# Optimization experiments

Measured on AMD Instinct MI355X. Metric: run time of the kernel, lower is better.

Reference implementation:

```python
import jax, jax.numpy as jnp
import numpy as np

NUM_GROUPS = 8
ROUTING_ITERS = 3
EPS = 1e-8

def setup_inputs() -> dict:
    key = jax.random.key(0)
    ks = jax.random.split(key, 6)
    B, C, H, W = 16, 256, 64, 64
    Cq = C // 4
    G = NUM_GROUPS
    x = jax.random.normal(ks[0], (B, C, H, W), jnp.float32)
    group_assignments = jax.random.uniform(ks[1], (B, C, G), jnp.float32)
    conv_w = jax.random.normal(ks[2], (Cq, C), jnp.float32) * 0.05
    conv_b = jax.random.normal(ks[3], (Cq,), jnp.float32) * 0.05
    lin_w = jax.random.normal(ks[4], (C * G, Cq), jnp.float32) * 0.05
    lin_b = jax.random.normal(ks[5], (C * G,), jnp.float32) * 0.05
    return {"x": x, "group_assignments": group_assignments,
            "conv_w": conv_w, "conv_b": conv_b, "lin_w": lin_w, "lin_b": lin_b}

def reference(x, group_assignments, conv_w, conv_b, lin_w, lin_b):
    B, C, H, W = x.shape
    G = NUM_GROUPS
    # routing_predictor: 1x1 conv (pure channel mix) -> ReLU -> global avg pool -> linear
    h = jax.nn.relu(jnp.einsum('bchw,dc->bdhw', x, conv_w) + conv_b[None, :, None, None])
    pooled = h.mean(axis=(2, 3))                               # (B, C//4)
    logits = (pooled @ lin_w.T + lin_b).reshape(B, C, G)       # (B, C, G)
    logits = logits + jnp.log(group_assignments + EPS)
    xf = x.reshape(B, C, H * W)                                # (B, C, N)
    x_norm = jnp.maximum(jnp.linalg.norm(xf, axis=2), EPS)     # (B, C)
    # dynamic routing: last iteration's softmax/group-sum contributes nothing to output,
    # so only ROUTING_ITERS-1 agreement updates are applied (same math as torch code)
    for _ in range(ROUTING_ITERS - 1):
        w = jax.nn.softmax(logits, axis=-1)                    # (B, C, G)
        s = jnp.einsum('bcg,bcn->bgn', w, xf)                  # group outputs (B, G, N)
        s_norm = jnp.maximum(jnp.linalg.norm(s, axis=2), EPS)  # (B, G)
        sim = jnp.einsum('bcn,bgn->bcg', xf, s) / (x_norm[:, :, None] * s_norm[:, None, :])
        logits = logits + sim
    final_weights = jax.nn.softmax(logits, axis=-1)
    return final_weights, x
```

## Files before the change

### kernel.cpp

```cpp
#include <hip/hip_runtime.h>

#define BB 16
#define CC 256
#define NN 4096
#define CN (CC*NN)
#define GG 8
#define EPSF 1e-8f
#define NT 64

typedef __attribute__((ext_vector_type(8))) short bf16x8;
typedef __attribute__((ext_vector_type(4))) float f32x4;
typedef __attribute__((ext_vector_type(2))) unsigned int uint32x2;

__device__ __forceinline__ unsigned short bfr(float f) {
  unsigned int u = __float_as_uint(f);
  return (unsigned short)((u + 0x7FFFu + ((u >> 16) & 1u)) >> 16);
}

__global__ __launch_bounds__(512, 2) void k_prep(const float* __restrict__ x,
                                                 const float* __restrict__ conv_w,
                                                 const float* __restrict__ conv_b,
                                                 float* __restrict__ xout,
                                                 float* __restrict__ xnp,
                                                 float* __restrict__ pooledpart,
                                                 unsigned short* __restrict__ xbf_g) {
  const int b = blockIdx.x >> 6;
  const int chunk = blockIdx.x & 63;
  const int t = threadIdx.x;
  const int lane = t & 63, wv = t >> 6;
  __shared__ unsigned short xbf[16384];
  __shared__ float pool[8 * 16];

  const int dt = wv >> 1, h2 = wv & 1;
  const int g = lane >> 4, col = lane & 15;
  const int drow = dt * 16 + col;
  union AF { uint4 q; bf16x8 v; unsigned short u[8]; } a[8];
  {
    const float* wrow = conv_w + (size_t)drow * 256;
#pragma unroll
    for (int kk = 0; kk < 8; ++kk) {
      float4 w0 = *(const float4*)(wrow + kk * 32 + g * 8);
      float4 w1 = *(const float4*)(wrow + kk * 32 + g * 8 + 4);
      a[kk].u[0] = bfr(w0.x); a[kk].u[1] = bfr(w0.y);
      a[kk].u[2] = bfr(w0.z); a[kk].u[3] = bfr(w0.w);
      a[kk].u[4] = bfr(w1.x); a[kk].u[5] = bfr(w1.y);
      a[kk].u[6] = bfr(w1.z); a[kk].u[7] = bfr(w1.w);
    }
  }

  const float* xb = x + (size_t)b * CN + chunk * NT;
  const int r0 = t >> 4, j = t & 15;
  f32x4 v[8];
  float sq[8];
#pragma unroll
  for (int k = 0; k < 8; ++k)
    v[k] = *(const f32x4*)(xb + (size_t)(k * 32 + r0) * NN + j * 4);
#pragma unroll
  for (int k = 0; k < 8; ++k) {
    ushort4 hh;
    hh.x = bfr(v[k].x); hh.y = bfr(v[k].y); hh.z = bfr(v[k].z); hh.w = bfr(v[k].w);
    *(ushort4*)&xbf[(k * 4 + (j >> 2)) * 512 + r0 * 16 + (j & 3) * 4] = hh;
    sq[k] = v[k].x * v[k].x + v[k].y * v[k].y + v[k].z * v[k].z + v[k].w * v[k].w;
  }
  float* xo = xout + (size_t)b * CN + chunk * NT;
#pragma unroll
  for (int k = 0; k < 8; ++k)
    __builtin_nontemporal_store(v[k],
        (f32x4*)(xo + (size_t)(k * 32 + r0) * NN + j * 4));
#pragma unroll
  for (int k = 0; k < 8; ++k) {
    float s = sq[k];
    s += __shfl_xor(s, 1, 64); s += __shfl_xor(s, 2, 64);
    s += __shfl_xor(s, 4, 64); s += __shfl_xor(s, 8, 64);
    sq[k] = s;
  }
  if ((t & 15) == 0) {
    float* xp = xnp + ((size_t)b * 64 + chunk) * 256 + r0;
#pragma unroll
    for (int k = 0; k < 8; ++k) xp[k * 32] = sq[k];
  }
  __syncthreads();

  {
    uint4* xgo4 = (uint4*)(xbf_g + (size_t)(b * 64 + chunk) * 16384);
    const uint4* xl4 = (const uint4*)xbf;
#pragma unroll
    for (int k = 0; k < 4; ++k) xgo4[k * 512 + t] = xl4[k * 512 + t];
  }

  f32x4 acc0 = {0.f, 0.f, 0.f, 0.f}, acc1 = {0.f, 0.f, 0.f, 0.f};
  const unsigned int xbase = (unsigned int)(size_t)&xbf[0];
  const unsigned int lanoff = (unsigned int)(col * 2 + g * 256);
#pragma unroll
  for (int kk = 0; kk < 8; ++kk) {
    const unsigned int ra = xbase + (unsigned int)((kk * 4 + 2 * h2) * 1024) + lanoff;
    const unsigned int rb = ra + 1024;
    union BF { uint32x2 tr[2]; bf16x8 v; } b0, b1;
    asm volatile("ds_read_b64_tr_b16 %0, %1" : "=v"(b0.tr[0]) : "v"(ra));
    asm volatile("ds_read_b64_tr_b16 %0, %1" : "=v"(b0.tr[1]) : "v"(ra + 128));
    asm volatile("ds_read_b64_tr_b16 %0, %1" : "=v"(b1.tr[0]) : "v"(rb));
    asm volatile("ds_read_b64_tr_b16 %0, %1" : "=v"(b1.tr[1]) : "v"(rb + 128));
    asm volatile("s_waitcnt lgkmcnt(0)" ::: "memory");
    __builtin_amdgcn_sched_barrier(0);
    acc0 = __builtin_amdgcn_mfma_f32_16x16x32_bf16(a[kk].v, b0.v, acc0, 0, 0, 0);
    acc1 = __builtin_amdgcn_mfma_f32_16x16x32_bf16(a[kk].v, b1.v, acc1, 0, 0, 0);
  }
  const float4 bias = *(const float4*)(conv_b + dt * 16 + 4 * g);
  const float br[4] = {bias.x, bias.y, bias.z, bias.w};
  float hs[4];
#pragma unroll
  for (int r = 0; r < 4; ++r) {
    float hv = fmaxf(acc0[r] + br[r], 0.f) + fmaxf(acc1[r] + br[r], 0.f);
    hv += __shfl_xor(hv, 1, 64); hv += __shfl_xor(hv, 2, 64);
    hv += __shfl_xor(hv, 4, 64); hv += __shfl_xor(hv, 8, 64);
    hs[r] = hv;
  }
  if (col == 0) {
#pragma unroll
    for (int r = 0; r < 4; ++r) pool[wv * 16 + g * 4 + r] = hs[r];
  }
  __syncthreads();
  if (t < 64) {
    const int dtt = t >> 4, idx = t & 15;
    pooledpart[((size_t)b * 64 + chunk) * 64 + t] =
        pool[(dtt * 2) * 16 + idx] + pool[(dtt * 2 + 1) * 16 + idx];
  }
}

__global__ __launch_bounds__(256) void k_logits(const float* __restrict__ pooledpart,
                                                const float* __restrict__ lin_w,
                                                const float* __restrict__ lin_b,
                                                const float* __restrict__ ga,
                                                float* __restrict__ logits,
                                                unsigned short* __restrict__ wgT) {
  const int b = blockIdx.x, t = threadIdx.x;
  __shared__ float ps2[4][64];
  __shared__ float ps[64];
  {
    const int d = t & 63, q = t >> 6;
    float s = 0.f;
#pragma unroll
    for (int k = 0; k < 16; ++k)
      s += pooledpart[((size_t)b * 64 + q * 16 + k) * 64 + d];
    ps2[q][d] = s;
  }
  __syncthreads();
  if (t < 64) ps[t] = (ps2[0][t] + ps2[1][t] + ps2[2][t] + ps2[3][t]) * (1.f / 4096.f);
  __syncthreads();
  const int c = t;
  float out[8];
#pragma unroll
  for (int g = 0; g < 8; ++g) {
    const float4* wr = (const float4*)(lin_w + ((size_t)c * 8 + g) * 64);
    float s = 0.f;
#pragma unroll
    for (int k4 = 0; k4 < 16; ++k4) {
      float4 wv = wr[k4];
      s += wv.x * ps[k4 * 4] + wv.y * ps[k4 * 4 + 1] + wv.z * ps[k4 * 4 + 2] +
           wv.w * ps[k4 * 4 + 3];
    }
    out[g] = s + lin_b[c * 8 + g] + logf(ga[((size_t)b * 256 + c) * 8 + g] + EPSF);
  }
  float* lp = logits + ((size_t)b * 256 + c) * 8;
  *(float4*)lp = make_float4(out[0], out[1], out[2], out[3]);
  *(float4*)(lp + 4) = make_float4(out[4], out[5], out[6], out[7]);
  float m = out[0];
#pragma unroll
  for (int g = 1; g < 8; ++g) m = fmaxf(m, out[g]);
  float sum = 0.f;
#pragma unroll
  for (int g = 0; g < 8; ++g) { out[g] = __expf(out[g] - m); sum += out[g]; }
  float r = 1.f / sum;
  unsigned short* wb = wgT + (size_t)b * 4096;
#pragma unroll
  for (int g = 0; g < 8; ++g) wb[g * 256 + c] = bfr(out[g] * r);
#pragma unroll
  for (int g = 8; g < 16; ++g) wb[g * 256 + c] = 0;
}

__global__ __launch_bounds__(512) void k_route(const unsigned short* __restrict__ xbf_g,
                                               const unsigned short* __restrict__ wgT,
                                               float* __restrict__ spart2,
                                               float* __restrict__ simpart) {
  const int b = blockIdx.x >> 6;
  const int chunk = blockIdx.x & 63;
  const int t = threadIdx.x;
  const int lane = t & 63, wv = t >> 6;
  const int col = lane & 15, grp = lane >> 4;
  __shared__ unsigned short xbf[16384];
  __shared__ unsigned short stb[1024];
  __shared__ float spool[64];

  {
    const uint4* xg = (const uint4*)xbf_g + (size_t)(b * 64 + chunk) * 2048;
    uint4* xl = (uint4*)xbf;
#pragma unroll
    for (int k = 0; k < 4; ++k) xl[k * 512 + t] = xg[k * 512 + t];
  }
  __syncthreads();

  const unsigned int xbase = (unsigned int)(size_t)&xbf[0];
  const unsigned int sbase = (unsigned int)(size_t)&stb[0];
  const unsigned int lanoff = (unsigned int)(col * 2 + grp * 256);

  if (wv < 4) {
    const int nt = wv;
    union AF { uint4 q; bf16x8 v; } a[8];
    const uint4* wq = (const uint4*)(wgT + (size_t)b * 4096);
#pragma unroll
    for (int kk = 0; kk < 8; ++kk) a[kk].q = wq[col * 32 + kk * 4 + grp];
    f32x4 acc = {0.f, 0.f, 0.f, 0.f};
#pragma unroll
    for (int kk = 0; kk < 8; ++kk) {
      const unsigned int ra = xbase + (unsigned int)((kk * 4 + nt) * 1024) + lanoff;
      union BF { uint32x2 tr[2]; bf16x8 v; } bf;
      asm volatile("ds_read_b64_tr_b16 %0, %1" : "=v"(bf.tr[0]) : "v"(ra));
      asm volatile("ds_read_b64_tr_b16 %0, %1" : "=v"(bf.tr[1]) : "v"(ra + 128));
      asm volatile("s_waitcnt lgkmcnt(0)" ::: "memory");
      __builtin_amdgcn_sched_barrier(0);
      acc = __builtin_amdgcn_mfma_f32_16x16x32_bf16(a[kk].v, bf.v, acc, 0, 0, 0);
    }
    {
      ushort4 sv4;
      sv4.x = bfr(acc[0]); sv4.y = bfr(acc[1]); sv4.z = bfr(acc[2]); sv4.w = bfr(acc[3]);
      *(ushort4*)&stb[(nt >> 1) * 512 + ((nt & 1) * 16 + col) * 16 + 4 * grp] = sv4;
      float s2[4];
#pragma unroll
      for (int r = 0; r < 4; ++r) {
        float vv = acc[r] * acc[r];
        vv += __shfl_xor(vv, 1, 64); vv += __shfl_xor(vv, 2, 64);
        vv += __shfl_xor(vv, 4, 64); vv += __shfl_xor(vv, 8, 64);
        s2[r] = vv;
      }
      if (col == 0) {
#pragma unroll
        for (int r = 0; r < 4; ++r) spool[nt * 16 + 4 * grp + r] = s2[r];
      }
    }
  }
  __syncthreads();
  if (t < 8)
    spart2[((size_t)b * 64 + chunk) * 8 + t] =
        spool[t] + spool[16 + t] + spool[32 + t] + spool[48 + t];

  float* sp = simpart + ((size_t)b * 64 + chunk) * 2048;
#pragma unroll
  for (int m2 = 0; m2 < 2; ++m2) {
    const int mc = wv * 2 + m2;
    const int kkA = mc >> 1;
    const int rowin = (mc & 1) * 16 + col;
    f32x4 acc = {0.f, 0.f, 0.f, 0.f};
#pragma unroll
    for (int kh = 0; kh < 2; ++kh) {
      union AF { uint4 q; bf16x8 v; } aa;
      aa.q = *(const uint4*)&xbf[(kkA * 4 + kh * 2 + (grp >> 1)) * 512 + rowin * 16 +
                                 (grp & 1) * 8];
      const unsigned int rb = sbase + (unsigned int)(kh * 1024) + lanoff;
      union BF { uint32x2 tr[2]; bf16x8 v; } bs;
      asm volatile("ds_read_b64_tr_b16 %0, %1" : "=v"(bs.tr[0]) : "v"(rb));
      asm volatile("ds_read_b64_tr_b16 %0, %1" : "=v"(bs.tr[1]) : "v"(rb + 128));
      asm volatile("s_waitcnt lgkmcnt(0)" ::: "memory");
      __builtin_amdgcn_sched_barrier(0);
      acc = __builtin_amdgcn_mfma_f32_16x16x32_bf16(aa.v, bs.v, acc, 0, 0, 0);
    }
    if (col < 8) {
#pragma unroll
      for (int r = 0; r < 4; ++r)
        sp[(size_t)(mc * 16 + 4 * grp + r) * 8 + col] = acc[r];
    }
  }
}

template <int FINAL>
__global__ __launch_bounds__(256) void k_upd(const float* __restrict__ simpart,
                                             const float* __restrict__ xnp,
                                             const float* __restrict__ spart2,
                                             float* __restrict__ logits,
                                             float* __restrict__ xnorm,
                                             unsigned short* __restrict__ wgT,
                                             float* __restrict__ outw) {
  const int b = blockIdx.x >> 4;
  const int c0 = (blockIdx.x & 15) * 16;
  const int t = threadIdx.x;
  __shared__ float simld[16][8];
  __shared__ float xnl[16];
  __shared__ float snr8[8];
  {
    const int pair = t >> 1, kh = t & 1;
    const int cl = pair >> 3, g = pair & 7;
    float sm = 0.f;
    const float* sp = simpart + (((size_t)b * 64 + kh * 32) * 256 + c0 + cl) * 8 + g;
#pragma unroll 8
    for (int k = 0; k < 32; ++k) sm += sp[(size_t)k * 2048];
    sm += __shfl_xor(sm, 1, 64);
    if (kh == 0) simld[cl][g] = sm;
  }
  {
    const int cl2 = t >> 4, kq = t & 15;
    if (!FINAL) {
      float p = 0.f;
#pragma unroll
      for (int jj = 0; jj < 4; ++jj)
        p += xnp[((size_t)b * 64 + kq + 16 * jj) * 256 + c0 + cl2];
      p += __shfl_xor(p, 1, 64); p += __shfl_xor(p, 2, 64);
      p += __shfl_xor(p, 4, 64); p += __shfl_xor(p, 8, 64);
      if (kq == 0) {
        float xn = fmaxf(sqrtf(p), EPSF);
        xnl[cl2] = xn;
        xnorm[b * 256 + c0 + cl2] = xn;
      }
    } else {
      if (kq == 0) xnl[cl2] = xnorm[b * 256 + c0 + cl2];
    }
  }
  if (t < 64) {
    const int g2 = t >> 3, kq = t & 7;
    float p = 0.f;
#pragma unroll
    for (int jj = 0; jj < 8; ++jj) p += spart2[((size_t)b * 64 + kq + 8 * jj) * 8 + g2];
    p += __shfl_xor(p, 1, 64); p += __shfl_xor(p, 2, 64); p += __shfl_xor(p, 4, 64);
    if (kq == 0) snr8[g2] = 1.f / fmaxf(sqrtf(p), EPSF);
  }
  __syncthreads();
  if (t < 16) {
    const int c = c0 + t;
    float* lp = logits + ((size_t)b * 256 + c) * 8;
    float4 l0 = *(const float4*)lp, l1 = *(const float4*)(lp + 4);
    float lg[8] = {l0.x, l0.y, l0.z, l0.w, l1.x, l1.y, l1.z, l1.w};
    const float xni = 1.f / xnl[t];
#pragma unroll
    for (int g = 0; g < 8; ++g) lg[g] += simld[t][g] * xni * snr8[g];
    if (!FINAL) {
      *(float4*)lp = make_float4(lg[0], lg[1], lg[2], lg[3]);
      *(float4*)(lp + 4) = make_float4(lg[4], lg[5], lg[6], lg[7]);
    }
    float m = lg[0];
#pragma unroll
    for (int g = 1; g < 8; ++g) m = fmaxf(m, lg[g]);
    float sum = 0.f;
#pragma unroll
    for (int g = 0; g < 8; ++g) { lg[g] = __expf(lg[g] - m); sum += lg[g]; }
    float r = 1.f / sum;
    if (!FINAL) {
      unsigned short* wb = wgT + (size_t)b * 4096;
#pragma unroll
      for (int g = 0; g < 8; ++g) wb[g * 256 + c] = bfr(lg[g] * r);
#pragma unroll
      for (int g = 8; g < 16; ++g) wb[g * 256 + c] = 0;
    } else {
      float4* op = (float4*)(outw + ((size_t)b * 256 + c) * 8);
      op[0] = make_float4(lg[0] * r, lg[1] * r, lg[2] * r, lg[3] * r);
      op[1] = make_float4(lg[4] * r, lg[5] * r, lg[6] * r, lg[7] * r);
    }
  }
}

extern "C" void kernel_launch(void* const* d_in, const int* in_sizes, int n_in,
                              void* d_out, int out_size, void* d_ws, size_t ws_size,
                              hipStream_t stream) {
  const float* x = (const float*)d_in[0];
  const float* ga = (const float*)d_in[1];
  const float* conv_w = (const float*)d_in[2];
  const float* conv_b = (const float*)d_in[3];
  const float* lin_w = (const float*)d_in[4];
  const float* lin_b = (const float*)d_in[5];
  float* out = (float*)d_out;
  float* outx = out + 32768;

  float* ws = (float*)d_ws;
  float* pooledpart = ws;
  float* logits = ws + 81920;
  unsigned short* wgT = (unsigned short*)(ws + 114688);
  float* xnorm = ws + 147456;
  float* xnp = ws + 151552;
  float* spart2 = ws + 413696;
  float* simpart = ws + 421888;
  unsigned short* xbf_g = (unsigned short*)(ws + 2519040);

  k_prep<<<1024, 512, 0, stream>>>(x, conv_w, conv_b, outx, xnp, pooledpart, xbf_g);
  k_logits<<<16, 256, 0, stream>>>(pooledpart, lin_w, lin_b, ga, logits, wgT);

  k_route<<<1024, 512, 0, stream>>>(xbf_g, wgT, spart2, simpart);
  k_upd<0><<<256, 256, 0, stream>>>(simpart, xnp, spart2, logits, xnorm, wgT, out);

  k_route<<<1024, 512, 0, stream>>>(xbf_g, wgT, spart2, simpart);
  k_upd<1><<<256, 256, 0, stream>>>(simpart, xnp, spart2, logits, xnorm, wgT, out);
}
```

Baseline: 87.71 us.

## Split x passthrough copy and norm computation into separate kernel

Moves the fp32 output copy of x and the per-channel squared-norm reduction out of the prep kernel into a dedicated streaming kernel that reduces a whole row per block. The prep kernel now only converts to bf16 and runs the conv, and the update kernel reads a single precomputed sum instead of reducing 64 partials. This lightens the prep kernel's store and register load. In exchange, x is read from memory twice, relying on cache to absorb the second read.

```diff
diff --git a/kernel.cpp b/kernel.cpp
--- a/kernel.cpp
+++ b/kernel.cpp
@@ -17,11 +17,31 @@
   return (unsigned short)((u + 0x7FFFu + ((u >> 16) & 1u)) >> 16);
 }
 
+__global__ __launch_bounds__(256) void k_copy(const float* __restrict__ x,
+                                              float* __restrict__ xout,
+                                              float* __restrict__ xnsq) {
+  const int bc = blockIdx.x;
+  const int t = threadIdx.x;
+  const float* xr = x + (size_t)bc * NN;
+  float* xw = xout + (size_t)bc * NN;
+  float s = 0.f;
+#pragma unroll
+  for (int jj = 0; jj < 4; ++jj) {
+    f32x4 v = *(const f32x4*)(xr + (jj * 256 + t) * 4);
+    __builtin_nontemporal_store(v, (f32x4*)(xw + (jj * 256 + t) * 4));
+    s += v.x * v.x + v.y * v.y + v.z * v.z + v.w * v.w;
+  }
+#pragma unroll
+  for (int off = 1; off < 64; off <<= 1) s += __shfl_xor(s, off, 64);
+  __shared__ float red[4];
+  if ((t & 63) == 0) red[t >> 6] = s;
+  __syncthreads();
+  if (t == 0) xnsq[bc] = red[0] + red[1] + red[2] + red[3];
+}
+
 __global__ __launch_bounds__(512, 2) void k_prep(const float* __restrict__ x,
                                                  const float* __restrict__ conv_w,
                                                  const float* __restrict__ conv_b,
-                                                 float* __restrict__ xout,
-                                                 float* __restrict__ xnp,
                                                  float* __restrict__ pooledpart,
                                                  unsigned short* __restrict__ xbf_g) {
   const int b = blockIdx.x >> 6;
@@ -51,7 +71,6 @@
   const float* xb = x + (size_t)b * CN + chunk * NT;
   const int r0 = t >> 4, j = t & 15;
   f32x4 v[8];
-  float sq[8];
 #pragma unroll
   for (int k = 0; k < 8; ++k)
     v[k] = *(const f32x4*)(xb + (size_t)(k * 32 + r0) * NN + j * 4);
@@ -60,24 +79,6 @@
     ushort4 hh;
     hh.x = bfr(v[k].x); hh.y = bfr(v[k].y); hh.z = bfr(v[k].z); hh.w = bfr(v[k].w);
     *(ushort4*)&xbf[(k * 4 + (j >> 2)) * 512 + r0 * 16 + (j & 3) * 4] = hh;
-    sq[k] = v[k].x * v[k].x + v[k].y * v[k].y + v[k].z * v[k].z + v[k].w * v[k].w;
-  }
-  float* xo = xout + (size_t)b * CN + chunk * NT;
-#pragma unroll
-  for (int k = 0; k < 8; ++k)
-    __builtin_nontemporal_store(v[k],
-        (f32x4*)(xo + (size_t)(k * 32 + r0) * NN + j * 4));
-#pragma unroll
-  for (int k = 0; k < 8; ++k) {
-    float s = sq[k];
-    s += __shfl_xor(s, 1, 64); s += __shfl_xor(s, 2, 64);
-    s += __shfl_xor(s, 4, 64); s += __shfl_xor(s, 8, 64);
-    sq[k] = s;
-  }
-  if ((t & 15) == 0) {
-    float* xp = xnp + ((size_t)b * 64 + chunk) * 256 + r0;
-#pragma unroll
-    for (int k = 0; k < 8; ++k) xp[k * 32] = sq[k];
   }
   __syncthreads();
 
@@ -273,7 +274,7 @@
 
 template <int FINAL>
 __global__ __launch_bounds__(256) void k_upd(const float* __restrict__ simpart,
-                                             const float* __restrict__ xnp,
+                                             const float* __restrict__ xnsq,
                                              const float* __restrict__ spart2,
                                              float* __restrict__ logits,
                                              float* __restrict__ xnorm,
@@ -297,20 +298,14 @@
   }
   {
     const int cl2 = t >> 4, kq = t & 15;
-    if (!FINAL) {
-      float p = 0.f;
-#pragma unroll
-      for (int jj = 0; jj < 4; ++jj)
-        p += xnp[((size_t)b * 64 + kq + 16 * jj) * 256 + c0 + cl2];
-      p += __shfl_xor(p, 1, 64); p += __shfl_xor(p, 2, 64);
-      p += __shfl_xor(p, 4, 64); p += __shfl_xor(p, 8, 64);
-      if (kq == 0) {
-        float xn = fmaxf(sqrtf(p), EPSF);
+    if (kq == 0) {
+      if (!FINAL) {
+        float xn = fmaxf(sqrtf(xnsq[(size_t)b * 256 + c0 + cl2]), EPSF);
         xnl[cl2] = xn;
         xnorm[b * 256 + c0 + cl2] = xn;
+      } else {
+        xnl[cl2] = xnorm[b * 256 + c0 + cl2];
       }
-    } else {
-      if (kq == 0) xnl[cl2] = xnorm[b * 256 + c0 + cl2];
     }
   }
   if (t < 64) {
@@ -372,17 +367,18 @@
   float* logits = ws + 81920;
   unsigned short* wgT = (unsigned short*)(ws + 114688);
   float* xnorm = ws + 147456;
-  float* xnp = ws + 151552;
+  float* xnsq = ws + 151552;
   float* spart2 = ws + 413696;
   float* simpart = ws + 421888;
   unsigned short* xbf_g = (unsigned short*)(ws + 2519040);
 
-  k_prep<<<1024, 512, 0, stream>>>(x, conv_w, conv_b, outx, xnp, pooledpart, xbf_g);
+  k_copy<<<4096, 256, 0, stream>>>(x, outx, xnsq);
+  k_prep<<<1024, 512, 0, stream>>>(x, conv_w, conv_b, pooledpart, xbf_g);
   k_logits<<<16, 256, 0, stream>>>(pooledpart, lin_w, lin_b, ga, logits, wgT);
 
   k_route<<<1024, 512, 0, stream>>>(xbf_g, wgT, spart2, simpart);
-  k_upd<0><<<256, 256, 0, stream>>>(simpart, xnp, spart2, logits, xnorm, wgT, out);
+  k_upd<0><<<256, 256, 0, stream>>>(simpart, xnsq, spart2, logits, xnorm, wgT, out);
 
   k_route<<<1024, 512, 0, stream>>>(xbf_g, wgT, spart2, simpart);
-  k_upd<1><<<256, 256, 0, stream>>>(simpart, xnp, spart2, logits, xnorm, wgT, out);
-}
+  k_upd<1><<<256, 256, 0, stream>>>(simpart, xnsq, spart2, logits, xnorm, wgT, out);
+}
```

Result: slower. 100.8 us (+15.0%).
